# Kernel optimization log

Hardware: AMD Instinct MI355X
Metric: run time of the kernel (lower is better)

The kernel has to match this reference:

```python
import jax, jax.numpy as jnp
import numpy as np

B, S, F = 64, 4096, 128      # batch, seq_len, fcnn_unit
RANK, FUSED = 16, 10


def setup_inputs() -> dict:
    key = jax.random.key(0)
    ks = jax.random.split(key, 10)
    xavier = lambda k, shape: jax.random.normal(k, shape, jnp.float32) * np.sqrt(2.0 / (shape[-2] + shape[-1]))
    return {
        "imu_h": jax.random.normal(ks[0], (B, S, F), jnp.float32),
        "vid_h": jax.random.normal(ks[1], (B, S, F), jnp.float32),
        "anthro": jax.random.uniform(ks[2], (B, 1, 2), jnp.float32, 0.5, 1.5),
        "imu_factor": xavier(ks[3], (RANK, 1, F + 1, FUSED)),
        "vid_factor": xavier(ks[4], (RANK, 1, F + 1, FUSED)),
        "fusion_weights": xavier(ks[5], (1, RANK)),
        "fusion_bias": jnp.zeros((1, FUSED), jnp.float32),
        "W1": xavier(ks[6], (FUSED, F)),
        "b1": jnp.zeros((F,), jnp.float32),
        "W2": xavier(ks[7], (F, 2)),
        "b2": jnp.zeros((2,), jnp.float32),
    }


def reference(imu_h, vid_h, anthro, imu_factor, vid_factor,
              fusion_weights, fusion_bias, W1, b1, W2, b2):
    b, s, _ = imu_h.shape
    ones = jnp.ones((b, s, 1), imu_h.dtype)
    _imu_h = jnp.concatenate([ones, imu_h], axis=2)   # [B,S,F+1]
    _vid_h = jnp.concatenate([ones, vid_h], axis=2)
    # torch.matmul([B,S,F+1], [rank,1,F+1,d]) -> [rank,B,S,d]
    fusion_imu = jnp.einsum('bsf,rfd->rbsd', _imu_h, imu_factor[:, 0])
    fusion_vid = jnp.einsum('bsf,rfd->rbsd', _vid_h, vid_factor[:, 0])
    fusion_zy = fusion_imu * fusion_vid               # [rank,B,S,d]
    # weighted combine over rank + bias -> [B,S,d]
    seq = jnp.einsum('r,rbsd->bsd', fusion_weights[0], fusion_zy) + fusion_bias[0]
    seq = jax.nn.relu(seq @ W1 + b1)                  # [B,S,F]
    seq = seq @ W2 + b2                               # [B,S,2]
    wh = (anthro[:, 0, 0] * anthro[:, 0, 1])[:, None, None]  # weight*height
    return seq / wh
```

## Files before the change

### kernel.cpp

```cpp
#include <hip/hip_runtime.h>
#include <hip/hip_bf16.h>
#include <stdint.h>


#define NTOK   262144
#define FDIM   128
#define RANKN  16
#define FUSED  10
#define WTE    (FUSED*RANKN*FDIM)

typedef unsigned short u16;
typedef __bf16 bf16x8 __attribute__((ext_vector_type(8)));
typedef float  f32x4  __attribute__((ext_vector_type(4)));

static __device__ __forceinline__ u16 f2bf(float f) {
    union { float f; uint32_t u; } c; c.f = f;
    uint32_t u = c.u + 0x7FFFu + ((c.u >> 16) & 1u);
    return (u16)(u >> 16);
}

__global__ void prep_kernel(const float* __restrict__ imf, const float* __restrict__ vif,
                            const float* __restrict__ fw,  const float* __restrict__ fb,
                            const float* __restrict__ W1,  const float* __restrict__ b1,
                            u16* __restrict__ wImu, u16* __restrict__ wVid,
                            float* __restrict__ a0, float* __restrict__ b0,
                            float* __restrict__ b1p) {
    int idx = blockIdx.x * blockDim.x + threadIdx.x;
    if (idx < FUSED * RANKN * FDIM) {
        int k = idx & 127;
        int r = (idx >> 7) & 15;
        int d = idx >> 11;
        int src = r * ((FDIM + 1) * FUSED) + (k + 1) * FUSED + d;
        int kk   = k >> 5;
        int quad = (k >> 3) & 3;
        int j    = k & 7;
        int lane = quad * 16 + r;
        int dst  = ((d * 4 + kk) * 64 + lane) * 8 + j;
        wImu[dst] = f2bf(fw[r] * imf[src]);
        wVid[dst] = f2bf(vif[src]);
    }
    if (idx < RANKN * FUSED) {
        int r = idx & 15, d = idx >> 4;
        int src = r * ((FDIM + 1) * FUSED) + d;
        a0[idx] = fw[r] * imf[src];
        b0[idx] = vif[src];
    }
    if (idx < FDIM) {
        float acc = b1[idx];
        #pragma unroll
        for (int d = 0; d < FUSED; ++d) acc += fb[d] * W1[d * FDIM + idx];
        b1p[idx] = acc;
    }
}

__launch_bounds__(1024, 1)
__global__ void fusion_main(const float* __restrict__ imu, const float* __restrict__ vid,
                            const float* __restrict__ anthro,
                            const u16* __restrict__ wImuG, const u16* __restrict__ wVidG,
                            const float* __restrict__ a0g, const float* __restrict__ b0g,
                            const float* __restrict__ W1g, const float* __restrict__ b1pg,
                            const float* __restrict__ W2g, const float* __restrict__ b2g,
                            float* __restrict__ out) {
    extern __shared__ char smem[];
    u16*   sFI  = (u16*)smem;
    u16*   sFV  = sFI + WTE;
    float* sA0  = (float*)(sFV + WTE);
    float* sB0  = sA0 + 160;
    float* sW1t = sB0 + 160;
    float* sB1  = sW1t + FDIM * 12;
    float* sW2  = sB1 + FDIM;

    {
        const uint4* srcI = (const uint4*)wImuG;
        const uint4* srcV = (const uint4*)wVidG;
        uint4* dstI = (uint4*)sFI;
        uint4* dstV = (uint4*)sFV;
        const int n16 = WTE * 2 / 16;
        for (int i = threadIdx.x; i < n16; i += blockDim.x) { dstI[i] = srcI[i]; dstV[i] = srcV[i]; }
    }
    for (int i = threadIdx.x; i < 160; i += blockDim.x) { sA0[i] = a0g[i]; sB0[i] = b0g[i]; }
    for (int i = threadIdx.x; i < FUSED * FDIM; i += blockDim.x) {
        int d = i >> 7, jc = i & 127;
        sW1t[jc * 12 + d] = W1g[i];
    }
    for (int i = threadIdx.x; i < FDIM; i += blockDim.x) sB1[i] = b1pg[i];
    for (int i = threadIdx.x; i < 256;  i += blockDim.x) sW2[i] = W2g[i];

    const int lane = threadIdx.x & 63;
    const int quad = lane >> 4;
    const int r16  = lane & 15;
    const int wid  = threadIdx.x >> 6;
    const int t0   = (blockIdx.x * 16 + wid) * 16;

    bf16x8 aI[4], aV[4];
    {
        const float* baseI = imu + (size_t)(t0 + r16) * FDIM + quad * 8;
        const float* baseV = vid + (size_t)(t0 + r16) * FDIM + quad * 8;
        #pragma unroll
        for (int kk = 0; kk < 4; ++kk) {
            f32x4 v0 = *(const f32x4*)(baseI + kk * 32);
            f32x4 v1 = *(const f32x4*)(baseI + kk * 32 + 4);
            f32x4 w0 = *(const f32x4*)(baseV + kk * 32);
            f32x4 w1 = *(const f32x4*)(baseV + kk * 32 + 4);
            bf16x8 a, b;
            #pragma unroll
            for (int j = 0; j < 4; ++j) {
                a[j]     = (__bf16)v0[j];
                a[j + 4] = (__bf16)v1[j];
                b[j]     = (__bf16)w0[j];
                b[j + 4] = (__bf16)w1[j];
            }
            aI[kk] = a;
            aV[kk] = b;
        }
    }
    __syncthreads();

    const bf16x8* fragI = (const bf16x8*)(const void*)sFI;
    const bf16x8* fragV = (const bf16x8*)(const void*)sFV;

    float seqv[4][FUSED];
    #pragma unroll
    for (int d = 0; d < FUSED; ++d) {
        f32x4 accU = {0.f, 0.f, 0.f, 0.f};
        f32x4 accV = {0.f, 0.f, 0.f, 0.f};
        #pragma unroll
        for (int kk = 0; kk < 4; ++kk) {
            bf16x8 bU = fragI[(d * 4 + kk) * 64 + lane];
            accU = __builtin_amdgcn_mfma_f32_16x16x32_bf16(aI[kk], bU, accU, 0, 0, 0);
            bf16x8 bV = fragV[(d * 4 + kk) * 64 + lane];
            accV = __builtin_amdgcn_mfma_f32_16x16x32_bf16(aV[kk], bV, accV, 0, 0, 0);
        }
        float a0v = sA0[d * RANKN + r16];
        float b0v = sB0[d * RANKN + r16];
        #pragma unroll
        for (int reg = 0; reg < 4; ++reg) {
            float p = (accU[reg] + a0v) * (accV[reg] + b0v);
            p += __shfl_xor(p, 1, 16);
            p += __shfl_xor(p, 2, 16);
            p += __shfl_xor(p, 4, 16);
            p += __shfl_xor(p, 8, 16);
            seqv[reg][d] = p;
        }
    }

    float o0[4] = {0.f, 0.f, 0.f, 0.f};
    float o1[4] = {0.f, 0.f, 0.f, 0.f};
    #pragma unroll
    for (int g = 0; g < 8; ++g) {
        const int jc = r16 + 16 * g;
        const float* wrow = sW1t + jc * 12;
        f32x4 wa = *(const f32x4*)wrow;
        f32x4 wb = *(const f32x4*)(wrow + 4);
        float w8 = wrow[8], w9 = wrow[9];
        float bb = sB1[jc];
        float w20 = sW2[jc * 2], w21 = sW2[jc * 2 + 1];
        #pragma unroll
        for (int reg = 0; reg < 4; ++reg) {
            float h = bb;
            #pragma unroll
            for (int d = 0; d < 4; ++d) h += seqv[reg][d] * wa[d];
            #pragma unroll
            for (int d = 0; d < 4; ++d) h += seqv[reg][4 + d] * wb[d];
            h += seqv[reg][8] * w8 + seqv[reg][9] * w9;
            float hr = fmaxf(h, 0.f);
            o0[reg] += hr * w20;
            o1[reg] += hr * w21;
        }
    }
    #pragma unroll
    for (int reg = 0; reg < 4; ++reg) {
        o0[reg] += __shfl_xor(o0[reg], 1, 16);
        o0[reg] += __shfl_xor(o0[reg], 2, 16);
        o0[reg] += __shfl_xor(o0[reg], 4, 16);
        o0[reg] += __shfl_xor(o0[reg], 8, 16);
        o1[reg] += __shfl_xor(o1[reg], 1, 16);
        o1[reg] += __shfl_xor(o1[reg], 2, 16);
        o1[reg] += __shfl_xor(o1[reg], 4, 16);
        o1[reg] += __shfl_xor(o1[reg], 8, 16);
    }

    const int bidx = t0 >> 12;
    const float invwh = 1.0f / (anthro[2 * bidx] * anthro[2 * bidx + 1]);
    const float b20 = b2g[0], b21 = b2g[1];
    if (r16 == 0) {
        #pragma unroll
        for (int reg = 0; reg < 4; ++reg) {
            const int t = t0 + quad * 4 + reg;
            float2 o = make_float2((o0[reg] + b20) * invwh, (o1[reg] + b21) * invwh);
            *(float2*)(out + 2 * t) = o;
        }
    }
}

extern "C" void kernel_launch(void* const* d_in, const int* in_sizes, int n_in,
                              void* d_out, int out_size, void* d_ws, size_t ws_size,
                              hipStream_t stream) {
    const float* imu    = (const float*)d_in[0];
    const float* vid    = (const float*)d_in[1];
    const float* anthro = (const float*)d_in[2];
    const float* imf    = (const float*)d_in[3];
    const float* vif    = (const float*)d_in[4];
    const float* fw     = (const float*)d_in[5];
    const float* fb     = (const float*)d_in[6];
    const float* W1     = (const float*)d_in[7];
    const float* b1     = (const float*)d_in[8];
    const float* W2     = (const float*)d_in[9];
    const float* b2     = (const float*)d_in[10];
    float* out = (float*)d_out;

    u16* wImu = (u16*)d_ws;
    u16* wVid = wImu + WTE;
    float* a0  = (float*)(wVid + WTE);
    float* b0  = a0 + 160;
    float* b1p = b0 + 160;

    prep_kernel<<<80, 256, 0, stream>>>(imf, vif, fw, fb, W1, b1, wImu, wVid, a0, b0, b1p);

    const size_t smem = (size_t)(2 * WTE) * sizeof(u16)
                      + (size_t)(160 + 160 + FDIM * 12 + FDIM + 256) * sizeof(float);
    fusion_main<<<1024, 1024, smem, stream>>>(imu, vid, anthro, wImu, wVid,
                                              a0, b0, W1, b1p, W2, b2, out);
}
```

Before: 357.4 us.

## Loop four token tiles per wave, swap MFMA operands, read small weights from global

The fusion kernel now uses 512 blocks of 512 threads, and each wave processes 64 tokens in four 16-token iterations instead of one tile. The per-block shared-memory factor copy is amortized over more tokens and blocks shrink to allow two per CU. MFMA operands are swapped so each lane's accumulator holds rank values for one token. This turns the rank reduction into two cross-quad shuffles and lets the MLP epilogue split hidden units across quads. The small W1, b1, W2 and bias tensors are re-laid out in the prep kernel and read straight from global/cache instead of shared memory. The trade-off is that input loads within a wave are now serialized across iterations, reducing memory-level parallelism.

```diff
diff --git a/kernel.cpp b/kernel.cpp
--- a/kernel.cpp
+++ b/kernel.cpp
@@ -22,9 +22,11 @@
 __global__ void prep_kernel(const float* __restrict__ imf, const float* __restrict__ vif,
                             const float* __restrict__ fw,  const float* __restrict__ fb,
                             const float* __restrict__ W1,  const float* __restrict__ b1,
+                            const float* __restrict__ W2,
                             u16* __restrict__ wImu, u16* __restrict__ wVid,
                             float* __restrict__ a0, float* __restrict__ b0,
-                            float* __restrict__ b1p) {
+                            float* __restrict__ b1p, float* __restrict__ W1q,
+                            float* __restrict__ w20, float* __restrict__ w21) {
     int idx = blockIdx.x * blockDim.x + threadIdx.x;
     if (idx < FUSED * RANKN * FDIM) {
         int k = idx & 127;
@@ -45,149 +47,138 @@
         a0[idx] = fw[r] * imf[src];
         b0[idx] = vif[src];
     }
+    if (idx < 1280) {
+        int w = idx & 31;
+        int t = idx >> 5;
+        int d = t % 10;
+        int q = t / 10;
+        W1q[idx] = W1[d * FDIM + q * 32 + w];
+    }
     if (idx < FDIM) {
         float acc = b1[idx];
         #pragma unroll
         for (int d = 0; d < FUSED; ++d) acc += fb[d] * W1[d * FDIM + idx];
         b1p[idx] = acc;
-    }
-}
-
-__launch_bounds__(1024, 1)
+        w20[idx] = W2[2 * idx];
+        w21[idx] = W2[2 * idx + 1];
+    }
+}
+
+__launch_bounds__(512, 2)
 __global__ void fusion_main(const float* __restrict__ imu, const float* __restrict__ vid,
                             const float* __restrict__ anthro,
                             const u16* __restrict__ wImuG, const u16* __restrict__ wVidG,
                             const float* __restrict__ a0g, const float* __restrict__ b0g,
-                            const float* __restrict__ W1g, const float* __restrict__ b1pg,
-                            const float* __restrict__ W2g, const float* __restrict__ b2g,
+                            const float* __restrict__ W1qg, const float* __restrict__ b1pg,
+                            const float* __restrict__ w20g, const float* __restrict__ w21g,
+                            const float* __restrict__ b2g,
                             float* __restrict__ out) {
     extern __shared__ char smem[];
-    u16*   sFI  = (u16*)smem;
-    u16*   sFV  = sFI + WTE;
-    float* sA0  = (float*)(sFV + WTE);
-    float* sB0  = sA0 + 160;
-    float* sW1t = sB0 + 160;
-    float* sB1  = sW1t + FDIM * 12;
-    float* sW2  = sB1 + FDIM;
+    u16* sFI = (u16*)smem;
+    u16* sFV = sFI + WTE;
 
     {
         const uint4* srcI = (const uint4*)wImuG;
         const uint4* srcV = (const uint4*)wVidG;
         uint4* dstI = (uint4*)sFI;
         uint4* dstV = (uint4*)sFV;
-        const int n16 = WTE * 2 / 16;
-        for (int i = threadIdx.x; i < n16; i += blockDim.x) { dstI[i] = srcI[i]; dstV[i] = srcV[i]; }
-    }
-    for (int i = threadIdx.x; i < 160; i += blockDim.x) { sA0[i] = a0g[i]; sB0[i] = b0g[i]; }
-    for (int i = threadIdx.x; i < FUSED * FDIM; i += blockDim.x) {
-        int d = i >> 7, jc = i & 127;
-        sW1t[jc * 12 + d] = W1g[i];
-    }
-    for (int i = threadIdx.x; i < FDIM; i += blockDim.x) sB1[i] = b1pg[i];
-    for (int i = threadIdx.x; i < 256;  i += blockDim.x) sW2[i] = W2g[i];
+        for (int i = threadIdx.x; i < WTE / 8; i += blockDim.x) {
+            dstI[i] = srcI[i];
+            dstV[i] = srcV[i];
+        }
+    }
+    __syncthreads();
 
     const int lane = threadIdx.x & 63;
     const int quad = lane >> 4;
     const int r16  = lane & 15;
     const int wid  = threadIdx.x >> 6;
-    const int t0   = (blockIdx.x * 16 + wid) * 16;
-
-    bf16x8 aI[4], aV[4];
-    {
-        const float* baseI = imu + (size_t)(t0 + r16) * FDIM + quad * 8;
-        const float* baseV = vid + (size_t)(t0 + r16) * FDIM + quad * 8;
-        #pragma unroll
-        for (int kk = 0; kk < 4; ++kk) {
-            f32x4 v0 = *(const f32x4*)(baseI + kk * 32);
-            f32x4 v1 = *(const f32x4*)(baseI + kk * 32 + 4);
-            f32x4 w0 = *(const f32x4*)(baseV + kk * 32);
-            f32x4 w1 = *(const f32x4*)(baseV + kk * 32 + 4);
-            bf16x8 a, b;
-            #pragma unroll
-            for (int j = 0; j < 4; ++j) {
-                a[j]     = (__bf16)v0[j];
-                a[j + 4] = (__bf16)v1[j];
-                b[j]     = (__bf16)w0[j];
-                b[j + 4] = (__bf16)w1[j];
-            }
-            aI[kk] = a;
-            aV[kk] = b;
-        }
-    }
-    __syncthreads();
+    const int wgl  = blockIdx.x * 8 + wid;
+    const int wbase = wgl * 64;
+
+    const int bidx = wbase >> 12;
+    const float invwh = 1.0f / (anthro[2 * bidx] * anthro[2 * bidx + 1]);
+    const float b20 = b2g[0], b21 = b2g[1];
 
     const bf16x8* fragI = (const bf16x8*)(const void*)sFI;
     const bf16x8* fragV = (const bf16x8*)(const void*)sFV;
 
-    float seqv[4][FUSED];
-    #pragma unroll
-    for (int d = 0; d < FUSED; ++d) {
-        f32x4 accU = {0.f, 0.f, 0.f, 0.f};
-        f32x4 accV = {0.f, 0.f, 0.f, 0.f};
+    for (int it = 0; it < 4; ++it) {
+        const int t0 = wbase + it * 16;
+
+        bf16x8 aI[4], aV[4];
+        {
+            const float* baseI = imu + (size_t)(t0 + r16) * FDIM + quad * 8;
+            #pragma unroll
+            for (int kk = 0; kk < 4; ++kk) {
+                f32x4 v0 = *(const f32x4*)(baseI + kk * 32);
+                f32x4 v1 = *(const f32x4*)(baseI + kk * 32 + 4);
+                bf16x8 a;
+                #pragma unroll
+                for (int j = 0; j < 4; ++j) { a[j] = (__bf16)v0[j]; a[j + 4] = (__bf16)v1[j]; }
+                aI[kk] = a;
+            }
+            const float* baseV = vid + (size_t)(t0 + r16) * FDIM + quad * 8;
+            #pragma unroll
+            for (int kk = 0; kk < 4; ++kk) {
+                f32x4 v0 = *(const f32x4*)(baseV + kk * 32);
+                f32x4 v1 = *(const f32x4*)(baseV + kk * 32 + 4);
+                bf16x8 a;
+                #pragma unroll
+                for (int j = 0; j < 4; ++j) { a[j] = (__bf16)v0[j]; a[j + 4] = (__bf16)v1[j]; }
+                aV[kk] = a;
+            }
+        }
+
+        float seqv[FUSED];
         #pragma unroll
-        for (int kk = 0; kk < 4; ++kk) {
-            bf16x8 bU = fragI[(d * 4 + kk) * 64 + lane];
-            accU = __builtin_amdgcn_mfma_f32_16x16x32_bf16(aI[kk], bU, accU, 0, 0, 0);
-            bf16x8 bV = fragV[(d * 4 + kk) * 64 + lane];
-            accV = __builtin_amdgcn_mfma_f32_16x16x32_bf16(aV[kk], bV, accV, 0, 0, 0);
-        }
-        float a0v = sA0[d * RANKN + r16];
-        float b0v = sB0[d * RANKN + r16];
+        for (int d = 0; d < FUSED; ++d) {
+            f32x4 accU = {0.f, 0.f, 0.f, 0.f};
+            f32x4 accV = {0.f, 0.f, 0.f, 0.f};
+            #pragma unroll
+            for (int kk = 0; kk < 4; ++kk) {
+                accU = __builtin_amdgcn_mfma_f32_16x16x32_bf16(fragI[(d * 4 + kk) * 64 + lane], aI[kk], accU, 0, 0, 0);
+                accV = __builtin_amdgcn_mfma_f32_16x16x32_bf16(fragV[(d * 4 + kk) * 64 + lane], aV[kk], accV, 0, 0, 0);
+            }
+            f32x4 a0c = *(const f32x4*)(a0g + d * 16 + quad * 4);
+            f32x4 b0c = *(const f32x4*)(b0g + d * 16 + quad * 4);
+            float s = 0.f;
+            #pragma unroll
+            for (int reg = 0; reg < 4; ++reg)
+                s += (accU[reg] + a0c[reg]) * (accV[reg] + b0c[reg]);
+            s += __shfl_xor(s, 16, 64);
+            s += __shfl_xor(s, 32, 64);
+            seqv[d] = s;
+        }
+
+        float o0 = 0.f, o1 = 0.f;
         #pragma unroll
-        for (int reg = 0; reg < 4; ++reg) {
-            float p = (accU[reg] + a0v) * (accV[reg] + b0v);
-            p += __shfl_xor(p, 1, 16);
-            p += __shfl_xor(p, 2, 16);
-            p += __shfl_xor(p, 4, 16);
-            p += __shfl_xor(p, 8, 16);
-            seqv[reg][d] = p;
-        }
-    }
-
-    float o0[4] = {0.f, 0.f, 0.f, 0.f};
-    float o1[4] = {0.f, 0.f, 0.f, 0.f};
-    #pragma unroll
-    for (int g = 0; g < 8; ++g) {
-        const int jc = r16 + 16 * g;
-        const float* wrow = sW1t + jc * 12;
-        f32x4 wa = *(const f32x4*)wrow;
-        f32x4 wb = *(const f32x4*)(wrow + 4);
-        float w8 = wrow[8], w9 = wrow[9];
-        float bb = sB1[jc];
-        float w20 = sW2[jc * 2], w21 = sW2[jc * 2 + 1];
-        #pragma unroll
-        for (int reg = 0; reg < 4; ++reg) {
-            float h = bb;
-            #pragma unroll
-            for (int d = 0; d < 4; ++d) h += seqv[reg][d] * wa[d];
-            #pragma unroll
-            for (int d = 0; d < 4; ++d) h += seqv[reg][4 + d] * wb[d];
-            h += seqv[reg][8] * w8 + seqv[reg][9] * w9;
-            float hr = fmaxf(h, 0.f);
-            o0[reg] += hr * w20;
-            o1[reg] += hr * w21;
-        }
-    }
-    #pragma unroll
-    for (int reg = 0; reg < 4; ++reg) {
-        o0[reg] += __shfl_xor(o0[reg], 1, 16);
-        o0[reg] += __shfl_xor(o0[reg], 2, 16);
-        o0[reg] += __shfl_xor(o0[reg], 4, 16);
-        o0[reg] += __shfl_xor(o0[reg], 8, 16);
-        o1[reg] += __shfl_xor(o1[reg], 1, 16);
-        o1[reg] += __shfl_xor(o1[reg], 2, 16);
-        o1[reg] += __shfl_xor(o1[reg], 4, 16);
-        o1[reg] += __shfl_xor(o1[reg], 8, 16);
-    }
-
-    const int bidx = t0 >> 12;
-    const float invwh = 1.0f / (anthro[2 * bidx] * anthro[2 * bidx + 1]);
-    const float b20 = b2g[0], b21 = b2g[1];
-    if (r16 == 0) {
-        #pragma unroll
-        for (int reg = 0; reg < 4; ++reg) {
-            const int t = t0 + quad * 4 + reg;
-            float2 o = make_float2((o0[reg] + b20) * invwh, (o1[reg] + b21) * invwh);
+        for (int g = 0; g < 8; ++g) {
+            const int jb = quad * 32 + g * 4;
+            f32x4 h = *(const f32x4*)(b1pg + jb);
+            #pragma unroll
+            for (int d = 0; d < FUSED; ++d) {
+                f32x4 wv = *(const f32x4*)(W1qg + (quad * 10 + d) * 32 + g * 4);
+                #pragma unroll
+                for (int i = 0; i < 4; ++i) h[i] += seqv[d] * wv[i];
+            }
+            f32x4 w20v = *(const f32x4*)(w20g + jb);
+            f32x4 w21v = *(const f32x4*)(w21g + jb);
+            #pragma unroll
+            for (int i = 0; i < 4; ++i) {
+                float hr = fmaxf(h[i], 0.f);
+                o0 += hr * w20v[i];
+                o1 += hr * w21v[i];
+            }
+        }
+        o0 += __shfl_xor(o0, 16, 64);
+        o0 += __shfl_xor(o0, 32, 64);
+        o1 += __shfl_xor(o1, 16, 64);
+        o1 += __shfl_xor(o1, 32, 64);
+
+        if (lane < 16) {
+            const int t = t0 + r16;
+            float2 o = make_float2((o0 + b20) * invwh, (o1 + b21) * invwh);
             *(float2*)(out + 2 * t) = o;
         }
     }
@@ -214,11 +205,14 @@
     float* a0  = (float*)(wVid + WTE);
     float* b0  = a0 + 160;
     float* b1p = b0 + 160;
-
-    prep_kernel<<<80, 256, 0, stream>>>(imf, vif, fw, fb, W1, b1, wImu, wVid, a0, b0, b1p);
-
-    const size_t smem = (size_t)(2 * WTE) * sizeof(u16)
-                      + (size_t)(160 + 160 + FDIM * 12 + FDIM + 256) * sizeof(float);
-    fusion_main<<<1024, 1024, smem, stream>>>(imu, vid, anthro, wImu, wVid,
-                                              a0, b0, W1, b1p, W2, b2, out);
-}
+    float* W1q = b1p + 128;
+    float* w20 = W1q + 1280;
+    float* w21 = w20 + 128;
+
+    prep_kernel<<<80, 256, 0, stream>>>(imf, vif, fw, fb, W1, b1, W2,
+                                        wImu, wVid, a0, b0, b1p, W1q, w20, w21);
+
+    const size_t smem = (size_t)(2 * WTE) * sizeof(u16);
+    fusion_main<<<512, 512, smem, stream>>>(imu, vid, anthro, wImu, wVid,
+                                            a0, b0, W1q, b1p, w20, w21, b2, out);
+}
```

Result: slower. 1.230 ms (+244.1%).
